# Optimization experiments

Hardware: AMD Instinct MI355X
Metric: run time of the kernel (lower is better)

Reference implementation:

```python
import jax, jax.numpy as jnp
import numpy as np

N, M, E, C, F, K = 10000, 20000, 160000, 128, 128, 3
R_CORRECTION = 1.0  # UpsampleModule passes 1 to DPOConv


def setup_inputs() -> dict:
    key = jax.random.key(0)
    ks = jax.random.split(key, 8)
    x = jax.random.normal(ks[0], (N, C), dtype=jnp.float32)
    pos = jax.random.uniform(ks[1], (N, 2), dtype=jnp.float32)
    pos_skip = jax.random.uniform(ks[2], (M, 2), dtype=jnp.float32)
    edge_index = jax.random.randint(ks[3], (2, E), 0, N, dtype=jnp.int64)
    W_conv = jax.random.normal(ks[4], (4 * C, F), dtype=jnp.float32) * 0.02
    b_conv = jnp.zeros((F,), dtype=jnp.float32)
    W2 = jax.random.normal(ks[5], (F, F), dtype=jnp.float32) * 0.02
    b2 = jnp.zeros((F,), dtype=jnp.float32)
    return {"x": x, "pos": pos, "pos_skip": pos_skip, "edge_index": edge_index,
            "W_conv": W_conv, "b_conv": b_conv, "W2": W2, "b2": b2}


def _dpo_conv(x, pos, edge_index, W_conv, b_conv):
    src, dst = edge_index[0], edge_index[1]  # PyG flow: j=source, i=target
    v_j, v_i = x[src], x[dst]                # [E, C]
    diff = pos[dst] - pos[src]               # pos_i - pos_j, [E, 2]
    r2 = jnp.sum(diff * diff, axis=-1)       # [E]
    scale = R_CORRECTION / (r2 + 0.01)       # [E]
    dx = diff[:, 0] * scale
    dy = diff[:, 1] * scale
    v_diff = v_i - v_j
    f = jnp.concatenate([v_diff * dx[:, None], v_diff * dy[:, None], v_j], axis=1)  # [E, 3C]
    agg = jax.ops.segment_sum(f, dst, num_segments=N)
    cnt = jax.ops.segment_sum(jnp.ones((E,), x.dtype), dst, num_segments=N)
    agg = agg / jnp.maximum(cnt, 1.0)[:, None]  # aggr='mean'
    h = jnp.concatenate([agg, x], axis=1) @ W_conv + b_conv  # [N, F]
    return h


def _knn_interpolate(h, pos, pos_skip, k):
    # squared distances target->source, [M, N]
    d2 = jnp.sum((pos_skip[:, None, :] - pos[None, :, :]) ** 2, axis=-1)
    neg_d, idx = jax.lax.top_k(-d2, k)         # k nearest, [M, k]
    w = 1.0 / jnp.maximum(-neg_d, 1e-16)       # inverse squared-distance weights
    return jnp.sum(w[:, :, None] * h[idx], axis=1) / jnp.sum(w, axis=1)[:, None]


def reference(x, pos, pos_skip, edge_index, W_conv, b_conv, W2, b2):
    h = _dpo_conv(x, pos, edge_index, W_conv, b_conv)
    h = jax.nn.elu(h)
    h = jax.nn.elu(h @ W2 + b2)
    return _knn_interpolate(h, pos, pos_skip, K)  # [M, F]
```

## Files before the change

### kernel.cpp

```cpp
#include <hip/hip_runtime.h>
#include <hip/hip_bf16.h>
#include <math.h>
#include <float.h>
#include <stdint.h>

#define N_NODES 10000
#define M_PTS   20000
#define E_EDGES 160000
#define C_CH    128
#define F_CH    128
#define G_GRID  64
#define N_CELLS (G_GRID*G_GRID)
#define NPB     16
#define ECAP    64
#define CCAP    24
#define A_STRIDE 520
#define H_STRIDE 136
#define N_TILES (N_NODES / NPB)
#define W1SZ (4*C_CH*F_CH)
#define W2SZ (F_CH*F_CH)

typedef __attribute__((ext_vector_type(8))) short short8;
typedef __attribute__((ext_vector_type(4))) float f32x4;

__device__ inline ushort f2bf(float v) {
    __hip_bfloat16 b = __float2bfloat16(v);
    return *reinterpret_cast<ushort*>(&b);
}
__device__ inline float bf2f(ushort u) {
    __hip_bfloat16 b = *reinterpret_cast<__hip_bfloat16*>(&u);
    return __bfloat162float(b);
}
__device__ inline float eluf(float v) { return (v > 0.f) ? v : expm1f(v); }
__device__ inline void insert3(uint64_t key, uint64_t& k0, uint64_t& k1, uint64_t& k2) {
    bool lt2 = key < k2, lt1 = key < k1, lt0 = key < k0;
    k2 = lt1 ? k1 : (lt2 ? key : k2);
    k1 = lt0 ? k0 : (lt1 ? key : k1);
    k0 = lt0 ? key : k0;
}

__global__ __launch_bounds__(256) void build_kernel(const int* __restrict__ ei,
    const float* __restrict__ pos, int* __restrict__ ecur, int* __restrict__ ccur,
    int4* __restrict__ edata, int4* __restrict__ cdata,
    const float* __restrict__ Wc, const float* __restrict__ W2,
    ushort* __restrict__ Wct_h, ushort* __restrict__ Wct_l,
    ushort* __restrict__ W2t_h, ushort* __restrict__ W2t_l)
{
    int i = blockIdx.x * 256 + threadIdx.x;
    if (i < E_EDGES) {
        int src = ei[i];
        int dst = ei[E_EDGES + i];
        float dxv = pos[2*dst]     - pos[2*src];
        float dyv = pos[2*dst + 1] - pos[2*src + 1];
        float r2 = dxv*dxv + dyv*dyv;
        float scale = 1.0f / (r2 + 0.01f);
        int slot = atomicAdd(&ecur[dst], 1);
        if (slot < ECAP)
            edata[dst*ECAP + slot] = make_int4(src, __float_as_int(dxv*scale),
                                               __float_as_int(dyv*scale), 0);
    } else if (i < E_EDGES + N_NODES) {
        int j = i - E_EDGES;
        float px = pos[2*j], py = pos[2*j+1];
        int cx = min(max((int)(px * G_GRID), 0), G_GRID - 1);
        int cy = min(max((int)(py * G_GRID), 0), G_GRID - 1);
        int c = cy * G_GRID + cx;
        int slot = atomicAdd(&ccur[c], 1);
        if (slot < CCAP)
            cdata[c*CCAP + slot] = make_int4(__float_as_int(px), __float_as_int(py), j, 0);
    } else if (i < E_EDGES + N_NODES + W1SZ) {
        int j = i - (E_EDGES + N_NODES);
        int n = j >> 9, k = j & 511;
        float v = Wc[k*F_CH + n];
        ushort h = f2bf(v);
        Wct_h[j] = h;
        Wct_l[j] = f2bf(v - bf2f(h));
    } else if (i < E_EDGES + N_NODES + W1SZ + W2SZ) {
        int j = i - (E_EDGES + N_NODES + W1SZ);
        int n = j >> 7, k = j & 127;
        float v = W2[k*F_CH + n];
        ushort h = f2bf(v);
        W2t_h[j] = h;
        W2t_l[j] = f2bf(v - bf2f(h));
    }
}

__global__ __launch_bounds__(512) void agg_gemm_kernel(const float* __restrict__ x,
    const int* __restrict__ ecur, const int4* __restrict__ edata,
    const ushort* __restrict__ Wct_h, const ushort* __restrict__ Wct_l,
    const ushort* __restrict__ W2t_h, const ushort* __restrict__ W2t_l,
    const float* __restrict__ bc, const float* __restrict__ b2,
    float* __restrict__ h2out)
{
    __shared__ alignas(16) ushort sA_h[NPB * A_STRIDE];
    __shared__ alignas(16) ushort sA_l[NPB * A_STRIDE];
    __shared__ alignas(16) ushort sH_h[NPB * H_STRIDE];
    __shared__ alignas(16) ushort sH_l[NPB * H_STRIDE];

    const int tid = threadIdx.x;
    const int lane = tid & 63;
    const int wave = tid >> 6;
    const int nodeBase = blockIdx.x * NPB;
    const float2* xv = (const float2*)x;

    for (int rr = wave*2; rr < wave*2 + 2; rr++) {
        int node = nodeBase + rr;
        float2 xi = xv[(size_t)node*64 + lane];
        int cnt = ecur[node];
        int m = min(cnt, ECAP);
        const int4* eb = edata + node*ECAP;
        float a1x = 0.f, a1y = 0.f, a2x = 0.f, a2y = 0.f, a3x = 0.f, a3y = 0.f;
        int p = 0;
        for (; p + 3 < m; p += 4) {
            int4 e0 = eb[p], e1 = eb[p+1], e2 = eb[p+2], e3 = eb[p+3];
            float2 x0 = xv[(size_t)e0.x*64 + lane];
            float2 x1 = xv[(size_t)e1.x*64 + lane];
            float2 x2 = xv[(size_t)e2.x*64 + lane];
            float2 x3 = xv[(size_t)e3.x*64 + lane];
            float dx0 = __int_as_float(e0.y), dy0 = __int_as_float(e0.z);
            float dx1 = __int_as_float(e1.y), dy1 = __int_as_float(e1.z);
            float dx2 = __int_as_float(e2.y), dy2 = __int_as_float(e2.z);
            float dx3 = __int_as_float(e3.y), dy3 = __int_as_float(e3.z);
            a1x = fmaf(xi.x - x0.x, dx0, a1x); a1y = fmaf(xi.y - x0.y, dx0, a1y);
            a2x = fmaf(xi.x - x0.x, dy0, a2x); a2y = fmaf(xi.y - x0.y, dy0, a2y);
            a3x += x0.x; a3y += x0.y;
            a1x = fmaf(xi.x - x1.x, dx1, a1x); a1y = fmaf(xi.y - x1.y, dx1, a1y);
            a2x = fmaf(xi.x - x1.x, dy1, a2x); a2y = fmaf(xi.y - x1.y, dy1, a2y);
            a3x += x1.x; a3y += x1.y;
            a1x = fmaf(xi.x - x2.x, dx2, a1x); a1y = fmaf(xi.y - x2.y, dx2, a1y);
            a2x = fmaf(xi.x - x2.x, dy2, a2x); a2y = fmaf(xi.y - x2.y, dy2, a2y);
            a3x += x2.x; a3y += x2.y;
            a1x = fmaf(xi.x - x3.x, dx3, a1x); a1y = fmaf(xi.y - x3.y, dx3, a1y);
            a2x = fmaf(xi.x - x3.x, dy3, a2x); a2y = fmaf(xi.y - x3.y, dy3, a2y);
            a3x += x3.x; a3y += x3.y;
        }
        for (; p < m; p++) {
            int4 e = eb[p];
            float2 xj = xv[(size_t)e.x*64 + lane];
            float dxe = __int_as_float(e.y), dye = __int_as_float(e.z);
            a1x = fmaf(xi.x - xj.x, dxe, a1x); a1y = fmaf(xi.y - xj.y, dxe, a1y);
            a2x = fmaf(xi.x - xj.x, dye, a2x); a2y = fmaf(xi.y - xj.y, dye, a2y);
            a3x += xj.x; a3y += xj.y;
        }
        float inv = 1.0f / fmaxf((float)cnt, 1.0f);
        float vals[4][2] = {{a1x*inv, a1y*inv}, {a2x*inv, a2y*inv},
                            {a3x*inv, a3y*inv}, {xi.x, xi.y}};
        int b = rr * A_STRIDE;
        int c0 = 2*lane;
        #pragma unroll
        for (int seg = 0; seg < 4; seg++) {
            ushort hx = f2bf(vals[seg][0]), hy = f2bf(vals[seg][1]);
            ushort lx = f2bf(vals[seg][0] - bf2f(hx)), ly = f2bf(vals[seg][1] - bf2f(hy));
            *(uint*)&sA_h[b + seg*128 + c0] = (uint)hx | ((uint)hy << 16);
            *(uint*)&sA_l[b + seg*128 + c0] = (uint)lx | ((uint)ly << 16);
        }
    }
    __syncthreads();

    const int col16 = lane & 15;
    const int quad  = lane >> 4;
    const int row   = col16;
    const int ncol  = wave*16 + col16;
    const float bcv = bc[ncol];
    const float b2v = b2[ncol];

    f32x4 acc = {0,0,0,0};
    for (int ks = 0; ks < 16; ks++) {
        int kb = ks*32 + quad*8;
        short8 ah = *(const short8*)&sA_h[row*A_STRIDE + kb];
        short8 al = *(const short8*)&sA_l[row*A_STRIDE + kb];
        short8 bh = *(const short8*)(Wct_h + (size_t)ncol*512 + kb);
        short8 bl = *(const short8*)(Wct_l + (size_t)ncol*512 + kb);
        acc = __builtin_amdgcn_mfma_f32_16x16x32_bf16(ah, bh, acc, 0, 0, 0);
        acc = __builtin_amdgcn_mfma_f32_16x16x32_bf16(ah, bl, acc, 0, 0, 0);
        acc = __builtin_amdgcn_mfma_f32_16x16x32_bf16(al, bh, acc, 0, 0, 0);
    }
    #pragma unroll
    for (int r = 0; r < 4; r++) {
        int rr = quad*4 + r;
        float v = eluf(acc[r] + bcv);
        ushort hh = f2bf(v);
        sH_h[rr*H_STRIDE + ncol] = hh;
        sH_l[rr*H_STRIDE + ncol] = f2bf(v - bf2f(hh));
    }
    __syncthreads();

    f32x4 acc2 = {0,0,0,0};
    for (int ks = 0; ks < 4; ks++) {
        int kb = ks*32 + quad*8;
        short8 ah = *(const short8*)&sH_h[row*H_STRIDE + kb];
        short8 al = *(const short8*)&sH_l[row*H_STRIDE + kb];
        short8 bh = *(const short8*)(W2t_h + ncol*128 + kb);
        short8 bl = *(const short8*)(W2t_l + ncol*128 + kb);
        acc2 = __builtin_amdgcn_mfma_f32_16x16x32_bf16(ah, bh, acc2, 0, 0, 0);
        acc2 = __builtin_amdgcn_mfma_f32_16x16x32_bf16(ah, bl, acc2, 0, 0, 0);
        acc2 = __builtin_amdgcn_mfma_f32_16x16x32_bf16(al, bh, acc2, 0, 0, 0);
    }
    #pragma unroll
    for (int r = 0; r < 4; r++) {
        int node = nodeBase + quad*4 + r;
        float v = eluf(acc2[r] + b2v);
        h2out[(size_t)node*F_CH + ncol] = v;
    }
}

__global__ __launch_bounds__(256) void knn_gather_kernel(const float* __restrict__ pos_skip,
    const int* __restrict__ ccur, const int4* __restrict__ cdata,
    const float* __restrict__ h2, float* __restrict__ out)
{
    int gt = blockIdx.x * 256 + threadIdx.x;
    if (gt >= M_PTS*8) return;
    int t = gt >> 3;
    int sub = gt & 7;
    float tx = pos_skip[2*t], ty = pos_skip[2*t+1];
    const float h = 1.0f / G_GRID;
    int cx = min(max((int)(tx * G_GRID), 0), G_GRID - 1);
    int cy = min(max((int)(ty * G_GRID), 0), G_GRID - 1);

    uint64_t k0 = UINT64_MAX, k1 = UINT64_MAX, k2 = UINT64_MAX;
    uint64_t m0 = UINT64_MAX, m1 = UINT64_MAX, m2 = UINT64_MAX;

    for (int r = 0; ; r++) {
        if (r > 0) {
            m0 = k0; m1 = k1; m2 = k2;
            #pragma unroll
            for (int m = 1; m <= 4; m <<= 1) {
                uint64_t p0 = __shfl_xor((unsigned long long)m0, m, 64);
                uint64_t p1 = __shfl_xor((unsigned long long)m1, m, 64);
                uint64_t p2 = __shfl_xor((unsigned long long)m2, m, 64);
                insert3(p0, m0, m1, m2);
                insert3(p1, m0, m1, m2);
                insert3(p2, m0, m1, m2);
            }
            float bound = ((r - 1) * h) * ((r - 1) * h) * 0.99999f;
            float d2cur = __uint_as_float((uint32_t)(m2 >> 32));
            if (d2cur < bound || r >= G_GRID) break;
        }
        int x0 = max(cx - r, 0), x1 = min(cx + r, G_GRID - 1);
        int y0 = max(cy - r, 0), y1 = min(cy + r, G_GRID - 1);
        int cidx = 0;
        for (int yy = y0; yy <= y1; yy++) {
            bool yedge = (yy == cy - r) || (yy == cy + r);
            for (int xx = x0; xx <= x1; xx++) {
                if (r > 0 && !yedge && xx != cx - r && xx != cx + r) continue;
                if ((cidx++ & 7) != sub) continue;
                int c = yy * G_GRID + xx;
                int pc = min(ccur[c], CCAP);
                const int4* cb = cdata + c*CCAP;
                for (int p = 0; p < pc; p++) {
                    int4 sp = cb[p];
                    float ddx = __fadd_rn(__int_as_float(sp.x), -tx);
                    float ddy = __fadd_rn(__int_as_float(sp.y), -ty);
                    float dd = __fadd_rn(__fmul_rn(ddx, ddx), __fmul_rn(ddy, ddy));
                    uint64_t key = ((uint64_t)__float_as_uint(dd) << 32) | (uint32_t)sp.z;
                    insert3(key, k0, k1, k2);
                }
            }
        }
    }

    float d0 = __uint_as_float((uint32_t)(m0 >> 32));
    float d1 = __uint_as_float((uint32_t)(m1 >> 32));
    float d2 = __uint_as_float((uint32_t)(m2 >> 32));
    float w0 = 1.0f / fmaxf(d0, 1e-16f);
    float w1 = 1.0f / fmaxf(d1, 1e-16f);
    float w2 = 1.0f / fmaxf(d2, 1e-16f);
    float wsum = w0 + w1 + w2;
    w0 /= wsum; w1 /= wsum; w2 /= wsum;
    int j0 = (int)(uint32_t)m0, j1 = (int)(uint32_t)m1, j2 = (int)(uint32_t)m2;
    const float4* r0 = (const float4*)(h2 + (size_t)j0*F_CH);
    const float4* r1 = (const float4*)(h2 + (size_t)j1*F_CH);
    const float4* r2 = (const float4*)(h2 + (size_t)j2*F_CH);
    float4* ot = (float4*)(out + (size_t)t*F_CH);
    #pragma unroll
    for (int q = 0; q < 4; q++) {
        int idx = sub*4 + q;
        float4 a = r0[idx], b = r1[idx], c = r2[idx];
        float4 v;
        v.x = w0*a.x + w1*b.x + w2*c.x;
        v.y = w0*a.y + w1*b.y + w2*c.y;
        v.z = w0*a.z + w1*b.z + w2*c.z;
        v.w = w0*a.w + w1*b.w + w2*c.w;
        ot[idx] = v;
    }
}

extern "C" void kernel_launch(void* const* d_in, const int* in_sizes, int n_in,
                              void* d_out, int out_size, void* d_ws, size_t ws_size,
                              hipStream_t stream) {
    const float* x        = (const float*)d_in[0];
    const float* pos      = (const float*)d_in[1];
    const float* pos_skip = (const float*)d_in[2];
    const int*   ei       = (const int*)  d_in[3];
    const float* Wc       = (const float*)d_in[4];
    const float* bc       = (const float*)d_in[5];
    const float* W2       = (const float*)d_in[6];
    const float* b2       = (const float*)d_in[7];
    float* out = (float*)d_out;

    char* ws = (char*)d_ws;
    size_t off = 0;
    auto alloc = [&](size_t bytes) {
        void* p = ws + off;
        off = (off + bytes + 255) & ~(size_t)255;
        return p;
    };
    int*    ecur   = (int*)   alloc((size_t)N_NODES * 4);
    int*    ccur   = (int*)   alloc((size_t)N_CELLS * 4);
    size_t  cur_bytes = (size_t)((char*)ccur - (char*)ecur) + (size_t)N_CELLS * 4;
    int4*   edata  = (int4*)  alloc((size_t)N_NODES * ECAP * 16);
    int4*   cdata  = (int4*)  alloc((size_t)N_CELLS * CCAP * 16);
    float*  h2     = (float*) alloc((size_t)N_NODES * F_CH * 4);
    ushort* Wct_h  = (ushort*)alloc((size_t)F_CH * 512 * 2);
    ushort* Wct_l  = (ushort*)alloc((size_t)F_CH * 512 * 2);
    ushort* W2t_h  = (ushort*)alloc((size_t)F_CH * 128 * 2);
    ushort* W2t_l  = (ushort*)alloc((size_t)F_CH * 128 * 2);

    hipMemsetAsync(ecur, 0, cur_bytes, stream);
    const int TOT = E_EDGES + N_NODES + W1SZ + W2SZ;
    build_kernel<<<(TOT + 255) / 256, 256, 0, stream>>>(ei, pos, ecur, ccur, edata, cdata,
                                                        Wc, W2, Wct_h, Wct_l, W2t_h, W2t_l);
    agg_gemm_kernel<<<N_TILES, 512, 0, stream>>>(x, ecur, edata,
        Wct_h, Wct_l, W2t_h, W2t_l, bc, b2, h2);
    knn_gather_kernel<<<(M_PTS*8 + 255) / 256, 256, 0, stream>>>(pos_skip, ccur, cdata, h2, out);
}
```

Before: 163.0 us.

## Use one wave per node in aggregation with 1024-thread blocks and fp64 accumulators

Doubles the block to 1024 threads so each of the 16 waves aggregates a single node instead of two, giving more memory-level parallelism for the gathered neighbour rows. Only the first 8 waves run the two MFMA GEMM stages; the other 8 sit idle through those phases. The per-edge accumulators change from float FMAs to double additions, which improves accuracy but costs slow FP64 adds and more registers. The launch bound of 1024 with a minimum-blocks hint may cap registers per thread.

Result: no change. 165.4 us (+1.5%).

```diff
diff --git a/kernel.cpp b/kernel.cpp
--- a/kernel.cpp
+++ b/kernel.cpp
@@ -84,7 +84,7 @@
     }
 }
 
-__global__ __launch_bounds__(512) void agg_gemm_kernel(const float* __restrict__ x,
+__global__ __launch_bounds__(1024, 8) void agg_gemm_kernel(const float* __restrict__ x,
     const int* __restrict__ ecur, const int4* __restrict__ edata,
     const ushort* __restrict__ Wct_h, const ushort* __restrict__ Wct_l,
     const ushort* __restrict__ W2t_h, const ushort* __restrict__ W2t_l,
@@ -102,13 +102,14 @@
     const int nodeBase = blockIdx.x * NPB;
     const float2* xv = (const float2*)x;
 
-    for (int rr = wave*2; rr < wave*2 + 2; rr++) {
+    {
+        const int rr = wave;
         int node = nodeBase + rr;
         float2 xi = xv[(size_t)node*64 + lane];
         int cnt = ecur[node];
         int m = min(cnt, ECAP);
         const int4* eb = edata + node*ECAP;
-        float a1x = 0.f, a1y = 0.f, a2x = 0.f, a2y = 0.f, a3x = 0.f, a3y = 0.f;
+        double a1x = 0., a1y = 0., a2x = 0., a2y = 0., a3x = 0., a3y = 0.;
         int p = 0;
         for (; p + 3 < m; p += 4) {
             int4 e0 = eb[p], e1 = eb[p+1], e2 = eb[p+2], e3 = eb[p+3];
@@ -116,34 +117,41 @@
             float2 x1 = xv[(size_t)e1.x*64 + lane];
             float2 x2 = xv[(size_t)e2.x*64 + lane];
             float2 x3 = xv[(size_t)e3.x*64 + lane];
-            float dx0 = __int_as_float(e0.y), dy0 = __int_as_float(e0.z);
-            float dx1 = __int_as_float(e1.y), dy1 = __int_as_float(e1.z);
-            float dx2 = __int_as_float(e2.y), dy2 = __int_as_float(e2.z);
-            float dx3 = __int_as_float(e3.y), dy3 = __int_as_float(e3.z);
-            a1x = fmaf(xi.x - x0.x, dx0, a1x); a1y = fmaf(xi.y - x0.y, dx0, a1y);
-            a2x = fmaf(xi.x - x0.x, dy0, a2x); a2y = fmaf(xi.y - x0.y, dy0, a2y);
-            a3x += x0.x; a3y += x0.y;
-            a1x = fmaf(xi.x - x1.x, dx1, a1x); a1y = fmaf(xi.y - x1.y, dx1, a1y);
-            a2x = fmaf(xi.x - x1.x, dy1, a2x); a2y = fmaf(xi.y - x1.y, dy1, a2y);
-            a3x += x1.x; a3y += x1.y;
-            a1x = fmaf(xi.x - x2.x, dx2, a1x); a1y = fmaf(xi.y - x2.y, dx2, a1y);
-            a2x = fmaf(xi.x - x2.x, dy2, a2x); a2y = fmaf(xi.y - x2.y, dy2, a2y);
-            a3x += x2.x; a3y += x2.y;
-            a1x = fmaf(xi.x - x3.x, dx3, a1x); a1y = fmaf(xi.y - x3.y, dx3, a1y);
-            a2x = fmaf(xi.x - x3.x, dy3, a2x); a2y = fmaf(xi.y - x3.y, dy3, a2y);
-            a3x += x3.x; a3y += x3.y;
+            float dx0=__int_as_float(e0.y), dy0=__int_as_float(e0.z);
+            float dx1=__int_as_float(e1.y), dy1=__int_as_float(e1.z);
+            float dx2=__int_as_float(e2.y), dy2=__int_as_float(e2.z);
+            float dx3=__int_as_float(e3.y), dy3=__int_as_float(e3.z);
+            float vx0 = xi.x - x0.x, vy0 = xi.y - x0.y;
+            float vx1 = xi.x - x1.x, vy1 = xi.y - x1.y;
+            float vx2 = xi.x - x2.x, vy2 = xi.y - x2.y;
+            float vx3 = xi.x - x3.x, vy3 = xi.y - x3.y;
+            a1x += (double)(vx0*dx0); a1y += (double)(vy0*dx0);
+            a2x += (double)(vx0*dy0); a2y += (double)(vy0*dy0);
+            a3x += (double)x0.x;      a3y += (double)x0.y;
+            a1x += (double)(vx1*dx1); a1y += (double)(vy1*dx1);
+            a2x += (double)(vx1*dy1); a2y += (double)(vy1*dy1);
+            a3x += (double)x1.x;      a3y += (double)x1.y;
+            a1x += (double)(vx2*dx2); a1y += (double)(vy2*dx2);
+            a2x += (double)(vx2*dy2); a2y += (double)(vy2*dy2);
+            a3x += (double)x2.x;      a3y += (double)x2.y;
+            a1x += (double)(vx3*dx3); a1y += (double)(vy3*dx3);
+            a2x += (double)(vx3*dy3); a2y += (double)(vy3*dy3);
+            a3x += (double)x3.x;      a3y += (double)x3.y;
         }
         for (; p < m; p++) {
             int4 e = eb[p];
             float2 xj = xv[(size_t)e.x*64 + lane];
             float dxe = __int_as_float(e.y), dye = __int_as_float(e.z);
-            a1x = fmaf(xi.x - xj.x, dxe, a1x); a1y = fmaf(xi.y - xj.y, dxe, a1y);
-            a2x = fmaf(xi.x - xj.x, dye, a2x); a2y = fmaf(xi.y - xj.y, dye, a2y);
-            a3x += xj.x; a3y += xj.y;
+            float vx = xi.x - xj.x, vy = xi.y - xj.y;
+            a1x += (double)(vx*dxe); a1y += (double)(vy*dxe);
+            a2x += (double)(vx*dye); a2y += (double)(vy*dye);
+            a3x += (double)xj.x;     a3y += (double)xj.y;
         }
         float inv = 1.0f / fmaxf((float)cnt, 1.0f);
-        float vals[4][2] = {{a1x*inv, a1y*inv}, {a2x*inv, a2y*inv},
-                            {a3x*inv, a3y*inv}, {xi.x, xi.y}};
+        float vals[4][2] = {{(float)a1x*inv, (float)a1y*inv},
+                            {(float)a2x*inv, (float)a2y*inv},
+                            {(float)a3x*inv, (float)a3y*inv},
+                            {xi.x, xi.y}};
         int b = rr * A_STRIDE;
         int c0 = 2*lane;
         #pragma unroll
@@ -159,47 +167,51 @@
     const int col16 = lane & 15;
     const int quad  = lane >> 4;
     const int row   = col16;
-    const int ncol  = wave*16 + col16;
-    const float bcv = bc[ncol];
-    const float b2v = b2[ncol];
-
-    f32x4 acc = {0,0,0,0};
-    for (int ks = 0; ks < 16; ks++) {
-        int kb = ks*32 + quad*8;
-        short8 ah = *(const short8*)&sA_h[row*A_STRIDE + kb];
-        short8 al = *(const short8*)&sA_l[row*A_STRIDE + kb];
-        short8 bh = *(const short8*)(Wct_h + (size_t)ncol*512 + kb);
-        short8 bl = *(const short8*)(Wct_l + (size_t)ncol*512 + kb);
-        acc = __builtin_amdgcn_mfma_f32_16x16x32_bf16(ah, bh, acc, 0, 0, 0);
-        acc = __builtin_amdgcn_mfma_f32_16x16x32_bf16(ah, bl, acc, 0, 0, 0);
-        acc = __builtin_amdgcn_mfma_f32_16x16x32_bf16(al, bh, acc, 0, 0, 0);
-    }
-    #pragma unroll
-    for (int r = 0; r < 4; r++) {
-        int rr = quad*4 + r;
-        float v = eluf(acc[r] + bcv);
-        ushort hh = f2bf(v);
-        sH_h[rr*H_STRIDE + ncol] = hh;
-        sH_l[rr*H_STRIDE + ncol] = f2bf(v - bf2f(hh));
+    const int ncol  = (wave & 7)*16 + col16;
+
+    if (wave < 8) {
+        const float bcv = bc[ncol];
+        f32x4 acc = {0,0,0,0};
+        for (int ks = 0; ks < 16; ks++) {
+            int kb = ks*32 + quad*8;
+            short8 ah = *(const short8*)&sA_h[row*A_STRIDE + kb];
+            short8 al = *(const short8*)&sA_l[row*A_STRIDE + kb];
+            short8 bh = *(const short8*)(Wct_h + (size_t)ncol*512 + kb);
+            short8 bl = *(const short8*)(Wct_l + (size_t)ncol*512 + kb);
+            acc = __builtin_amdgcn_mfma_f32_16x16x32_bf16(ah, bh, acc, 0, 0, 0);
+            acc = __builtin_amdgcn_mfma_f32_16x16x32_bf16(ah, bl, acc, 0, 0, 0);
+            acc = __builtin_amdgcn_mfma_f32_16x16x32_bf16(al, bh, acc, 0, 0, 0);
+        }
+        #pragma unroll
+        for (int r = 0; r < 4; r++) {
+            int rr = quad*4 + r;
+            float v = eluf(acc[r] + bcv);
+            ushort hh = f2bf(v);
+            sH_h[rr*H_STRIDE + ncol] = hh;
+            sH_l[rr*H_STRIDE + ncol] = f2bf(v - bf2f(hh));
+        }
     }
     __syncthreads();
 
-    f32x4 acc2 = {0,0,0,0};
-    for (int ks = 0; ks < 4; ks++) {
-        int kb = ks*32 + quad*8;
-        short8 ah = *(const short8*)&sH_h[row*H_STRIDE + kb];
-        short8 al = *(const short8*)&sH_l[row*H_STRIDE + kb];
-        short8 bh = *(const short8*)(W2t_h + ncol*128 + kb);
-        short8 bl = *(const short8*)(W2t_l + ncol*128 + kb);
-        acc2 = __builtin_amdgcn_mfma_f32_16x16x32_bf16(ah, bh, acc2, 0, 0, 0);
-        acc2 = __builtin_amdgcn_mfma_f32_16x16x32_bf16(ah, bl, acc2, 0, 0, 0);
-        acc2 = __builtin_amdgcn_mfma_f32_16x16x32_bf16(al, bh, acc2, 0, 0, 0);
-    }
-    #pragma unroll
-    for (int r = 0; r < 4; r++) {
-        int node = nodeBase + quad*4 + r;
-        float v = eluf(acc2[r] + b2v);
-        h2out[(size_t)node*F_CH + ncol] = v;
+    if (wave < 8) {
+        const float b2v = b2[ncol];
+        f32x4 acc2 = {0,0,0,0};
+        for (int ks = 0; ks < 4; ks++) {
+            int kb = ks*32 + quad*8;
+            short8 ah = *(const short8*)&sH_h[row*H_STRIDE + kb];
+            short8 al = *(const short8*)&sH_l[row*H_STRIDE + kb];
+            short8 bh = *(const short8*)(W2t_h + ncol*128 + kb);
+            short8 bl = *(const short8*)(W2t_l + ncol*128 + kb);
+            acc2 = __builtin_amdgcn_mfma_f32_16x16x32_bf16(ah, bh, acc2, 0, 0, 0);
+            acc2 = __builtin_amdgcn_mfma_f32_16x16x32_bf16(ah, bl, acc2, 0, 0, 0);
+            acc2 = __builtin_amdgcn_mfma_f32_16x16x32_bf16(al, bh, acc2, 0, 0, 0);
+        }
+        #pragma unroll
+        for (int r = 0; r < 4; r++) {
+            int node = nodeBase + quad*4 + r;
+            float v = eluf(acc2[r] + b2v);
+            h2out[(size_t)node*F_CH + ncol] = v;
+        }
     }
 }
 
@@ -319,7 +331,7 @@
     const int TOT = E_EDGES + N_NODES + W1SZ + W2SZ;
     build_kernel<<<(TOT + 255) / 256, 256, 0, stream>>>(ei, pos, ecur, ccur, edata, cdata,
                                                         Wc, W2, Wct_h, Wct_l, W2t_h, W2t_l);
-    agg_gemm_kernel<<<N_TILES, 512, 0, stream>>>(x, ecur, edata,
+    agg_gemm_kernel<<<N_TILES, 1024, 0, stream>>>(x, ecur, edata,
         Wct_h, Wct_l, W2t_h, W2t_l, bc, b2, h2);
     knn_gather_kernel<<<(M_PTS*8 + 255) / 256, 256, 0, stream>>>(pos_skip, ccur, cdata, h2, out);
 }
```
